# Kernel optimization log

Hardware: AMD Instinct MI355X
Metric: run time of the kernel (lower is better)

## Reference

```python
import jax, jax.numpy as jnp
import numpy as np

C = 64            # multiplicity of 0e and 1o in in_irreps
N_NODES = 20000
N_EDGES = 320000
RAD_DIM = 8
HID = 64
NUM_IRREPS_OUT = 4 * C   # 2C x 0e + 2C x 1o -> 256 scalar weights
AVG_NUM_NEIGHBORS = 16.0


def setup_inputs() -> dict:
    key = jax.random.key(0)
    ks = jax.random.split(key, 10)
    node_feats = jax.random.normal(ks[0], (N_NODES, C + 3 * C), jnp.float32)
    vectors = jax.random.normal(ks[1], (N_EDGES, 3), jnp.float32)
    radial_embedding = jax.random.normal(ks[2], (N_EDGES, RAD_DIM), jnp.float32)
    senders = jax.random.randint(ks[3], (N_EDGES,), 0, N_NODES, jnp.int32)
    receivers = jax.random.randint(ks[4], (N_EDGES,), 0, N_NODES, jnp.int32)
    # e3nn-style MLP params (no bias), forward scales by 1/sqrt(fan_in)
    W0 = jax.random.normal(ks[5], (RAD_DIM, HID), jnp.float32)
    W1 = jax.random.normal(ks[6], (HID, HID), jnp.float32)
    W2 = jax.random.normal(ks[7], (HID, HID), jnp.float32)
    W3 = jax.random.normal(ks[8], (HID, NUM_IRREPS_OUT), jnp.float32)
    return {"node_feats": node_feats, "vectors": vectors,
            "radial_embedding": radial_embedding, "senders": senders,
            "receivers": receivers, "W0": W0, "W1": W1, "W2": W2, "W3": W3}


def _mlp(x, W0, W1, W2, W3):
    # MultiLayerPerceptron with gradient_normalization=1.0: scale by 1/sqrt(fan_in)
    h = jax.nn.silu(x @ W0 / jnp.sqrt(jnp.asarray(W0.shape[0], x.dtype)))
    h = jax.nn.silu(h @ W1 / jnp.sqrt(jnp.asarray(HID, x.dtype)))
    h = jax.nn.silu(h @ W2 / jnp.sqrt(jnp.asarray(HID, x.dtype)))
    return h @ W3 / jnp.sqrt(jnp.asarray(HID, x.dtype))


def reference(node_feats, vectors, radial_embedding, senders, receivers, W0, W1, W2, W3):
    n = node_feats.shape[0]
    s = node_feats[:, :C]                      # [N, C]  0e block
    v = node_feats[:, C:].reshape(n, C, 3)     # [N, C, 3]  1o block
    s_e = s[senders]                           # gather  [E, C]
    v_e = v[senders]                           # gather  [E, C, 3]
    # spherical harmonics l=1 of -vectors, normalized input, component norm
    r = -vectors
    Y = jnp.sqrt(3.0) * r / jnp.linalg.norm(r, axis=-1, keepdims=True)  # [E, 3]
    # CG tensor product filtered to target irreps (0e + 1o):
    tp_v = s_e[:, :, None] * Y[:, None, :]                 # 0e x 1o -> 1o  [E,C,3]
    tp_s = jnp.einsum('eci,ei->ec', v_e, Y) / jnp.sqrt(3.0)  # 1o x 1o -> 0e  [E,C]
    msg_s = jnp.concatenate([s_e, tp_s], axis=-1)          # [E, 2C]
    msg_v = jnp.concatenate([v_e, tp_v], axis=1)           # [E, 2C, 3]
    # per-irrep MLP gate from radial embedding
    mix = _mlp(radial_embedding, W0, W1, W2, W3)           # [E, 4C]
    msg_s = msg_s * mix[:, :2 * C]
    msg_v = msg_v * mix[:, 2 * C:, None]
    # scatter-add into receivers
    out_s = jnp.zeros((n, 2 * C), msg_s.dtype).at[receivers].add(msg_s)
    out_v = jnp.zeros((n, 2 * C, 3), msg_v.dtype).at[receivers].add(msg_v)
    out = jnp.concatenate([out_s, out_v.reshape(n, 6 * C)], axis=-1)
    return out / AVG_NUM_NEIGHBORS                         # [N, 512]
```

## Files before the change

kernel.cpp:

```cpp
#include <hip/hip_runtime.h>

typedef __attribute__((ext_vector_type(8))) short bf16x8;
typedef __attribute__((ext_vector_type(4))) float f32x4;

static __device__ __forceinline__ unsigned short f2bf(float f) {
    unsigned int u = __float_as_uint(f);
    unsigned int r = (u + 0x7fffu + ((u >> 16) & 1u)) >> 16;
    return (unsigned short)r;
}
static __device__ __forceinline__ float bf2f(unsigned short h) {
    return __uint_as_float(((unsigned int)h) << 16);
}

#define WP_TOTAL 26624

__global__ __launch_bounds__(256) void zero_kernel(int* __restrict__ p, int n)
{
    int i = blockIdx.x * 256 + threadIdx.x;
    if (i < n) p[i] = 0;
}

__global__ __launch_bounds__(256) void prep_kernel(
    const float* __restrict__ W0, const float* __restrict__ W1,
    const float* __restrict__ W2, const float* __restrict__ W3,
    unsigned short* __restrict__ Wp,
    const int* __restrict__ recv, int* __restrict__ cnt, int E)
{
    int o = blockIdx.x * 256 + threadIdx.x;
    if (o < WP_TOTAL) {
        float val;
        if (o < 2048) {
            int nt = o >> 9, w = o & 511, lane = w >> 3, j = w & 7;
            int k = (lane >> 4) * 8 + j, n = nt * 16 + (lane & 15);
            val = (k < 8) ? W0[k * 64 + n] * 0.35355339059327373f : 0.f;
        } else if (o < 6144) {
            int oo = o - 2048, fid = oo >> 9, w = oo & 511, lane = w >> 3, j = w & 7;
            int nt = fid >> 1, ks = fid & 1;
            int k = ks * 32 + (lane >> 4) * 8 + j, n = nt * 16 + (lane & 15);
            val = W1[k * 64 + n] * 0.125f;
        } else if (o < 10240) {
            int oo = o - 6144, fid = oo >> 9, w = oo & 511, lane = w >> 3, j = w & 7;
            int nt = fid >> 1, ks = fid & 1;
            int k = ks * 32 + (lane >> 4) * 8 + j, n = nt * 16 + (lane & 15);
            val = W2[k * 64 + n] * 0.125f;
        } else {
            int oo = o - 10240, fid = oo >> 9, w = oo & 511, lane = w >> 3, j = w & 7;
            int nt = fid >> 1, ks = fid & 1;
            int k = ks * 32 + (lane >> 4) * 8 + j, n = nt * 16 + (lane & 15);
            val = W3[k * 256 + n] * 0.125f;
        }
        Wp[o] = f2bf(val);
    }
    if (o < E) atomicAdd(&cnt[recv[o]], 1);
}

__global__ __launch_bounds__(1024) void scan_kernel(const int* __restrict__ cnt,
                                                    int* __restrict__ off,
                                                    int* __restrict__ cursor, int N)
{
    __shared__ int wsum[16];
    const int t = threadIdx.x, lane = t & 63, wv = t >> 6;
    const int per = (N + 1023) / 1024;
    const int base = t * per;
    int s = 0;
    for (int i = 0; i < per; ++i) { int idx = base + i; if (idx < N) s += cnt[idx]; }
    int inc = s;
    #pragma unroll
    for (int d = 1; d < 64; d <<= 1) {
        int v = __shfl_up(inc, d, 64);
        if (lane >= d) inc += v;
    }
    if (lane == 63) wsum[wv] = inc;
    __syncthreads();
    if (t == 0) {
        int run = 0;
        #pragma unroll
        for (int w = 0; w < 16; ++w) { int v = wsum[w]; wsum[w] = run; run += v; }
    }
    __syncthreads();
    int run = wsum[wv] + inc - s;
    for (int i = 0; i < per; ++i) {
        int idx = base + i;
        if (idx < N) { off[idx] = run; cursor[idx] = run; run += cnt[idx]; }
    }
    if (t == 1023) off[N] = wsum[15] + inc;
}

__global__ __launch_bounds__(256) void fill_kernel(
    const int*   __restrict__ recv,
    const int*   __restrict__ senders,
    const float* __restrict__ vectors,
    int* __restrict__ cursor,
    int* __restrict__ edge_of,
    int* __restrict__ snd_pos,
    float4* __restrict__ Y4,
    int E)
{
    int i = blockIdx.x * 256 + threadIdx.x;
    if (i < E) {
        int p = atomicAdd(&cursor[recv[i]], 1);
        edge_of[p] = i;
        snd_pos[p] = senders[i];
        float r0 = -vectors[(size_t)i * 3 + 0];
        float r1 = -vectors[(size_t)i * 3 + 1];
        float r2 = -vectors[(size_t)i * 3 + 2];
        float inv = rsqrtf(r0 * r0 + r1 * r1 + r2 * r2);
        const float s3 = 1.7320508075688772f;
        Y4[p] = make_float4(s3 * r0 * inv, s3 * r1 * inv, s3 * r2 * inv, 0.f);
    }
}

__global__ __launch_bounds__(256) void mlp_pos_kernel(
    const float* __restrict__ radial,
    const int* __restrict__ edge_of,
    const unsigned short* __restrict__ Wp,
    unsigned short* __restrict__ mix,
    int E)
{
    __shared__ __align__(16) unsigned short sW[10240];
    __shared__ __align__(16) unsigned short sH[4][1024];
    __shared__ __align__(16) unsigned short sM[4][16 * 68];

    const int t = threadIdx.x;
    {
        int4* dst = (int4*)sW;
        const int4* src = (const int4*)Wp;
        #pragma unroll
        for (int i = 0; i < 5; ++i) dst[t + i * 256] = src[t + i * 256];
    }
    __syncthreads();

    const int wv = t >> 6, l = t & 63;
    const int lrow = l & 15, quad = l >> 4;
    const int p0 = blockIdx.x * 64 + wv * 16;
    if (p0 >= E) return;

    unsigned short* H = sH[wv];
    unsigned short* M = sM[wv];

    bf16x8 afr = {0, 0, 0, 0, 0, 0, 0, 0};
    if (quad == 0) {
        int i = p0 + lrow; if (i >= E) i = E - 1;
        int e = edge_of[i];
        const float* rr = radial + (size_t)e * 8;
        float4 ra = *(const float4*)rr;
        float4 rb = *(const float4*)(rr + 4);
        afr[0] = (short)f2bf(ra.x); afr[1] = (short)f2bf(ra.y);
        afr[2] = (short)f2bf(ra.z); afr[3] = (short)f2bf(ra.w);
        afr[4] = (short)f2bf(rb.x); afr[5] = (short)f2bf(rb.y);
        afr[6] = (short)f2bf(rb.z); afr[7] = (short)f2bf(rb.w);
    }
    #pragma unroll
    for (int nt = 0; nt < 4; ++nt) {
        bf16x8 b = *(const bf16x8*)(sW + nt * 512 + l * 8);
        f32x4 z = {0.f, 0.f, 0.f, 0.f};
        f32x4 cf = __builtin_amdgcn_mfma_f32_16x16x32_bf16(afr, b, z, 0, 0, 0);
        #pragma unroll
        for (int r = 0; r < 4; ++r) {
            float v = cf[r];
            float h = v / (1.f + __expf(-v));
            int er = quad * 4 + r;
            int f  = nt * 16 + lrow;
            H[er * 64 + (f ^ ((er & 7) << 3))] = f2bf(h);
        }
    }

    #pragma unroll 1
    for (int L = 0; L < 2; ++L) {
        const unsigned short* WL = sW + 2048 + L * 4096;
        bf16x8 a[2];
        #pragma unroll
        for (int ks = 0; ks < 2; ++ks)
            a[ks] = *(const bf16x8*)(H + lrow * 64 + ((ks * 32 + quad * 8) ^ ((lrow & 7) << 3)));
        f32x4 cf[4];
        #pragma unroll
        for (int nt = 0; nt < 4; ++nt) { f32x4 z = {0.f,0.f,0.f,0.f}; cf[nt] = z; }
        #pragma unroll
        for (int ks = 0; ks < 2; ++ks) {
            #pragma unroll
            for (int nt = 0; nt < 4; ++nt) {
                bf16x8 b = *(const bf16x8*)(WL + (nt * 2 + ks) * 512 + l * 8);
                cf[nt] = __builtin_amdgcn_mfma_f32_16x16x32_bf16(a[ks], b, cf[nt], 0, 0, 0);
            }
        }
        #pragma unroll
        for (int nt = 0; nt < 4; ++nt) {
            #pragma unroll
            for (int r = 0; r < 4; ++r) {
                float v = cf[nt][r];
                float h = v / (1.f + __expf(-v));
                int er = quad * 4 + r;
                int f  = nt * 16 + lrow;
                H[er * 64 + (f ^ ((er & 7) << 3))] = f2bf(h);
            }
        }
    }

    bf16x8 a3[2];
    #pragma unroll
    for (int ks = 0; ks < 2; ++ks)
        a3[ks] = *(const bf16x8*)(H + lrow * 64 + ((ks * 32 + quad * 8) ^ ((lrow & 7) << 3)));

    const unsigned short* W3 = Wp + 10240;
    #pragma unroll 1
    for (int g = 0; g < 4; ++g) {
        f32x4 cf[4];
        #pragma unroll
        for (int np = 0; np < 4; ++np) { f32x4 z = {0.f,0.f,0.f,0.f}; cf[np] = z; }
        #pragma unroll
        for (int ks = 0; ks < 2; ++ks) {
            #pragma unroll
            for (int np = 0; np < 4; ++np) {
                int nt = g * 4 + np;
                bf16x8 b = *(const bf16x8*)(W3 + (nt * 2 + ks) * 512 + l * 8);
                cf[np] = __builtin_amdgcn_mfma_f32_16x16x32_bf16(a3[ks], b, cf[np], 0, 0, 0);
            }
        }
        #pragma unroll
        for (int np = 0; np < 4; ++np) {
            int c2 = np * 16 + lrow;
            #pragma unroll
            for (int r = 0; r < 4; ++r)
                M[(quad * 4 + r) * 68 + c2] = f2bf(cf[np][r]);
        }
        #pragma unroll
        for (int i = 0; i < 4; ++i) {
            int ri = i * 4 + quad;
            ushort4 v = *(const ushort4*)&M[ri * 68 + lrow * 4];
            if (p0 + ri < E)
                *(ushort4*)&mix[(size_t)(p0 + ri) * 256 + g * 64 + lrow * 4] = v;
        }
    }
}

__global__ __launch_bounds__(256) void gather_kernel(
    const float* __restrict__ node_feats,
    const int*   __restrict__ snd_pos,
    const float4* __restrict__ Y4,
    const int*   __restrict__ off,
    const unsigned short* __restrict__ mix,
    float* __restrict__ out, int N)
{
    int wid  = threadIdx.x >> 6;
    int lane = threadIdx.x & 63;
    int n = blockIdx.x * 4 + wid;
    if (n >= N) return;

    int beg = off[n], end = off[n + 1];

    float a0 = 0.f, a1 = 0.f;
    float b0 = 0.f, b1 = 0.f, b2 = 0.f;
    float c0 = 0.f, c1 = 0.f, c2 = 0.f;

    const float is3 = 0.5773502691896258f;

    #pragma unroll 4
    for (int i = beg; i < end; ++i) {
        int snd  = snd_pos[i];
        float4 Y = Y4[i];

        const float* nf = node_feats + (size_t)snd * 256;
        float s_e = nf[lane];
        float v0  = nf[64 + lane * 3 + 0];
        float v1  = nf[64 + lane * 3 + 1];
        float v2  = nf[64 + lane * 3 + 2];

        const unsigned short* m = mix + (size_t)i * 256;
        float m0 = bf2f(m[lane]);
        float m1 = bf2f(m[64 + lane]);
        float m2 = bf2f(m[128 + lane]);
        float m3 = bf2f(m[192 + lane]);

        float tp_s = (v0 * Y.x + v1 * Y.y + v2 * Y.z) * is3;

        a0 += s_e * m0;
        a1 += tp_s * m1;
        b0 += v0 * m2; b1 += v1 * m2; b2 += v2 * m2;
        float sm = s_e * m3;
        c0 += Y.x * sm; c1 += Y.y * sm; c2 += Y.z * sm;
    }

    float* o = out + (size_t)n * 512;
    const float kk = 0.0625f;
    o[lane]      = a0 * kk;
    o[64 + lane] = a1 * kk;
    o[128 + lane * 3 + 0] = b0 * kk;
    o[128 + lane * 3 + 1] = b1 * kk;
    o[128 + lane * 3 + 2] = b2 * kk;
    o[320 + lane * 3 + 0] = c0 * kk;
    o[320 + lane * 3 + 1] = c1 * kk;
    o[320 + lane * 3 + 2] = c2 * kk;
}

#define HID 64
__global__ __launch_bounds__(256) void mlp_kernel(
    const float* __restrict__ radial,
    const float* __restrict__ W0g, const float* __restrict__ W1g,
    const float* __restrict__ W2g, const float* __restrict__ W3g,
    unsigned short* __restrict__ mix, int e1)
{
    __shared__ float  sHf[HID * 256];
    __shared__ float4 sW4[1024];

    const int t = threadIdx.x;
    const int e = blockIdx.x * 256 + t;
    const bool valid = e < e1;

    if (t < 128) sW4[t] = ((const float4*)W0g)[t];
    __syncthreads();

    float x[8];
    if (valid) {
        float4 ra = ((const float4*)radial)[(size_t)e * 2 + 0];
        float4 rb = ((const float4*)radial)[(size_t)e * 2 + 1];
        x[0]=ra.x; x[1]=ra.y; x[2]=ra.z; x[3]=ra.w;
        x[4]=rb.x; x[5]=rb.y; x[6]=rb.z; x[7]=rb.w;
    } else {
        #pragma unroll
        for (int k = 0; k < 8; ++k) x[k] = 0.f;
    }

    float acc[64];
    #pragma unroll
    for (int j = 0; j < 64; ++j) acc[j] = 0.f;
    #pragma unroll
    for (int k = 0; k < 8; ++k) {
        #pragma unroll
        for (int jq = 0; jq < 16; ++jq) {
            float4 w = sW4[k * 16 + jq];
            acc[jq*4+0] = fmaf(x[k], w.x, acc[jq*4+0]);
            acc[jq*4+1] = fmaf(x[k], w.y, acc[jq*4+1]);
            acc[jq*4+2] = fmaf(x[k], w.z, acc[jq*4+2]);
            acc[jq*4+3] = fmaf(x[k], w.w, acc[jq*4+3]);
        }
    }
    #pragma unroll
    for (int j = 0; j < 64; ++j) {
        float v = acc[j] * 0.35355339059327373f;
        sHf[j * 256 + t] = v / (1.f + __expf(-v));
    }
    __syncthreads();
    #pragma unroll
    for (int i = 0; i < 4; ++i) sW4[t + i * 256] = ((const float4*)W1g)[t + i * 256];
    __syncthreads();

    #pragma unroll
    for (int j = 0; j < 64; ++j) acc[j] = 0.f;
    #pragma unroll 2
    for (int k = 0; k < 64; ++k) {
        float hk = sHf[k * 256 + t];
        #pragma unroll
        for (int jq = 0; jq < 16; ++jq) {
            float4 w = sW4[k * 16 + jq];
            acc[jq*4+0] = fmaf(hk, w.x, acc[jq*4+0]);
            acc[jq*4+1] = fmaf(hk, w.y, acc[jq*4+1]);
            acc[jq*4+2] = fmaf(hk, w.z, acc[jq*4+2]);
            acc[jq*4+3] = fmaf(hk, w.w, acc[jq*4+3]);
        }
    }
    __syncthreads();
    #pragma unroll
    for (int i = 0; i < 4; ++i) sW4[t + i * 256] = ((const float4*)W2g)[t + i * 256];
    #pragma unroll
    for (int j = 0; j < 64; ++j) {
        float v = acc[j] * 0.125f;
        sHf[j * 256 + t] = v / (1.f + __expf(-v));
    }
    __syncthreads();

    #pragma unroll
    for (int j = 0; j < 64; ++j) acc[j] = 0.f;
    #pragma unroll 2
    for (int k = 0; k < 64; ++k) {
        float hk = sHf[k * 256 + t];
        #pragma unroll
        for (int jq = 0; jq < 16; ++jq) {
            float4 w = sW4[k * 16 + jq];
            acc[jq*4+0] = fmaf(hk, w.x, acc[jq*4+0]);
            acc[jq*4+1] = fmaf(hk, w.y, acc[jq*4+1]);
            acc[jq*4+2] = fmaf(hk, w.z, acc[jq*4+2]);
            acc[jq*4+3] = fmaf(hk, w.w, acc[jq*4+3]);
        }
    }
    __syncthreads();
    #pragma unroll
    for (int j = 0; j < 64; ++j) {
        float v = acc[j] * 0.125f;
        sHf[j * 256 + t] = v / (1.f + __expf(-v));
    }

    unsigned short* mrow = mix + (size_t)e * 256;
    #pragma unroll 1
    for (int jt = 0; jt < 4; ++jt) {
        #pragma unroll
        for (int i = 0; i < 4; ++i) {
            int m = t + i * 256;
            sW4[m] = ((const float4*)W3g)[(m >> 4) * 64 + jt * 16 + (m & 15)];
        }
        __syncthreads();

        #pragma unroll
        for (int j = 0; j < 64; ++j) acc[j] = 0.f;
        #pragma unroll 2
        for (int k = 0; k < 64; ++k) {
            float hk = sHf[k * 256 + t];
            #pragma unroll
            for (int jq = 0; jq < 16; ++jq) {
                float4 w = sW4[k * 16 + jq];
                acc[jq*4+0] = fmaf(hk, w.x, acc[jq*4+0]);
                acc[jq*4+1] = fmaf(hk, w.y, acc[jq*4+1]);
                acc[jq*4+2] = fmaf(hk, w.z, acc[jq*4+2]);
                acc[jq*4+3] = fmaf(hk, w.w, acc[jq*4+3]);
            }
        }
        if (valid) {
            #pragma unroll
            for (int j4 = 0; j4 < 16; ++j4) {
                ushort4 u;
                u.x = f2bf(acc[j4*4+0] * 0.125f);
                u.y = f2bf(acc[j4*4+1] * 0.125f);
                u.z = f2bf(acc[j4*4+2] * 0.125f);
                u.w = f2bf(acc[j4*4+3] * 0.125f);
                *reinterpret_cast<ushort4*>(&mrow[jt * 64 + j4 * 4]) = u;
            }
        }
        __syncthreads();
    }
}

__global__ __launch_bounds__(256) void scatter_kernel(
    const float* __restrict__ node_feats,
    const float* __restrict__ vectors,
    const int*   __restrict__ senders,
    const int*   __restrict__ receivers,
    const unsigned short* __restrict__ mix,
    float* __restrict__ out, int e0, int e1)
{
    int wid  = threadIdx.x >> 6;
    int lane = threadIdx.x & 63;
    int e = e0 + blockIdx.x * 4 + wid;
    if (e >= e1) return;

    int snd = senders[e];
    int rcv = receivers[e];

    float r0 = -vectors[(size_t)e * 3 + 0];
    float r1 = -vectors[(size_t)e * 3 + 1];
    float r2 = -vectors[(size_t)e * 3 + 2];
    float inv = rsqrtf(r0 * r0 + r1 * r1 + r2 * r2);
    float Y0 = 1.7320508075688772f * r0 * inv;
    float Y1 = 1.7320508075688772f * r1 * inv;
    float Y2 = 1.7320508075688772f * r2 * inv;

    const float* nf = node_feats + (size_t)snd * 256;
    float s_e = nf[lane];
    float v0 = nf[64 + lane * 3 + 0];
    float v1 = nf[64 + lane * 3 + 1];
    float v2 = nf[64 + lane * 3 + 2];

    float tp_s = (v0 * Y0 + v1 * Y1 + v2 * Y2) * 0.5773502691896258f;

    const unsigned short* m = mix + (size_t)(e - e0) * 256;
    float m0 = bf2f(m[lane]), m1 = bf2f(m[64 + lane]);
    float m2 = bf2f(m[128 + lane]), m3 = bf2f(m[192 + lane]);

    float* orow = out + (size_t)rcv * 512;
    const float kk = 0.0625f;
    atomicAdd(&orow[lane],      s_e  * m0 * kk);
    atomicAdd(&orow[64 + lane], tp_s * m1 * kk);
    float mv = m2 * kk;
    atomicAdd(&orow[128 + lane * 3 + 0], v0 * mv);
    atomicAdd(&orow[128 + lane * 3 + 1], v1 * mv);
    atomicAdd(&orow[128 + lane * 3 + 2], v2 * mv);
    float ms = s_e * m3 * kk;
    atomicAdd(&orow[320 + lane * 3 + 0], Y0 * ms);
    atomicAdd(&orow[320 + lane * 3 + 1], Y1 * ms);
    atomicAdd(&orow[320 + lane * 3 + 2], Y2 * ms);
}

extern "C" void kernel_launch(void* const* d_in, const int* in_sizes, int n_in,
                              void* d_out, int out_size, void* d_ws, size_t ws_size,
                              hipStream_t stream)
{
    const float* node_feats = (const float*)d_in[0];
    const float* vectors    = (const float*)d_in[1];
    const float* radial     = (const float*)d_in[2];
    const int*   senders    = (const int*)d_in[3];
    const int*   receivers  = (const int*)d_in[4];
    const float* W0         = (const float*)d_in[5];
    const float* W1         = (const float*)d_in[6];
    const float* W2         = (const float*)d_in[7];
    const float* W3         = (const float*)d_in[8];
    float* out = (float*)d_out;

    const int E = in_sizes[3];
    const int N = in_sizes[0] / 256;

    size_t mix_bytes = (size_t)E * 256 * sizeof(unsigned short);
    size_t mix_al    = (mix_bytes + 255) & ~(size_t)255;
    size_t int_bytes = (size_t)(N + (N + 1) + N + E + E) * sizeof(int);
    size_t int_al    = (int_bytes + 255) & ~(size_t)255;
    size_t y4_bytes  = (size_t)E * sizeof(float4);
    size_t y4_al     = (y4_bytes + 255) & ~(size_t)255;
    size_t wp_bytes  = (size_t)WP_TOTAL * sizeof(unsigned short);
    size_t need      = mix_al + int_al + y4_al + wp_bytes;

    if (ws_size >= need) {
        unsigned short* mix = (unsigned short*)d_ws;
        int* cnt      = (int*)((char*)d_ws + mix_al);
        int* off      = cnt + N;
        int* cursor   = off + (N + 1);
        int* edge_of  = cursor + N;
        int* snd_pos  = edge_of + E;
        float4* Y4    = (float4*)((char*)d_ws + mix_al + int_al);
        unsigned short* Wp = (unsigned short*)((char*)d_ws + mix_al + int_al + y4_al);

        zero_kernel<<<dim3((N + 255) / 256), dim3(256), 0, stream>>>(cnt, N);

        prep_kernel<<<dim3((E + 255) / 256), dim3(256), 0, stream>>>(
            W0, W1, W2, W3, Wp, receivers, cnt, E);
        scan_kernel<<<dim3(1), dim3(1024), 0, stream>>>(cnt, off, cursor, N);
        fill_kernel<<<dim3((E + 255) / 256), dim3(256), 0, stream>>>(
            receivers, senders, vectors, cursor, edge_of, snd_pos, Y4, E);

        mlp_pos_kernel<<<dim3((E + 63) / 64), dim3(256), 0, stream>>>(
            radial, edge_of, Wp, mix, E);

        gather_kernel<<<dim3((N + 3) / 4), dim3(256), 0, stream>>>(
            node_feats, snd_pos, Y4, off, mix, out, N);
    } else {
        hipMemsetAsync(d_out, 0, (size_t)out_size * sizeof(float), stream);
        size_t per_edge = 256 * sizeof(unsigned short);
        long long chunk_ll = (long long)(ws_size / per_edge);
        int chunk = (chunk_ll > E) ? E : (int)chunk_ll;
        chunk &= ~255;
        if (chunk <= 0) chunk = 256;
        unsigned short* mix = (unsigned short*)d_ws;
        for (int s = 0; s < E; s += chunk) {
            int eend = s + chunk; if (eend > E) eend = E;
            int ne = eend - s;
            mlp_kernel<<<dim3((ne + 255) / 256), dim3(256), 0, stream>>>(
                radial + (size_t)s * 8, W0, W1, W2, W3, mix, ne);
            scatter_kernel<<<dim3((ne + 3) / 4), dim3(256), 0, stream>>>(
                node_feats, vectors, senders, receivers, mix, out, s, eend);
        }
    }
}
```

Before: 225.8 us.

## Interleave node features and gate weights per channel for vectorized gather loads

Adds a kernel that repacks node features into one float4 per node and channel (scalar plus three vector components). The MLP now writes the four gate values for each channel contiguously as a ushort4, dropping the shared-memory staging buffer. The gather kernel then issues one 16-byte node load and one 8-byte gate load per lane instead of several strided scalar loads. The cost is an extra repack pass over node features and added workspace, and the MLP output stores become narrower and strided.

```diff
diff --git a/kernel.cpp b/kernel.cpp
--- a/kernel.cpp
+++ b/kernel.cpp
@@ -18,6 +18,18 @@
 {
     int i = blockIdx.x * 256 + threadIdx.x;
     if (i < n) p[i] = 0;
+}
+
+__global__ __launch_bounds__(256) void nf4_kernel(
+    const float* __restrict__ nf, float4* __restrict__ nf4, int N)
+{
+    int idx = blockIdx.x * 256 + threadIdx.x;
+    if (idx < N * 64) {
+        int n = idx >> 6, c = idx & 63;
+        const float* row = nf + (size_t)n * 256;
+        nf4[idx] = make_float4(row[c], row[64 + c * 3 + 0],
+                               row[64 + c * 3 + 1], row[64 + c * 3 + 2]);
+    }
 }
 
 __global__ __launch_bounds__(256) void prep_kernel(
@@ -114,12 +126,11 @@
     const float* __restrict__ radial,
     const int* __restrict__ edge_of,
     const unsigned short* __restrict__ Wp,
-    unsigned short* __restrict__ mix,
+    unsigned short* __restrict__ mix4,
     int E)
 {
     __shared__ __align__(16) unsigned short sW[10240];
     __shared__ __align__(16) unsigned short sH[4][1024];
-    __shared__ __align__(16) unsigned short sM[4][16 * 68];
 
     const int t = threadIdx.x;
     {
@@ -136,7 +147,6 @@
     if (p0 >= E) return;
 
     unsigned short* H = sH[wv];
-    unsigned short* M = sM[wv];
 
     bf16x8 afr = {0, 0, 0, 0, 0, 0, 0, 0};
     if (quad == 0) {
@@ -203,42 +213,39 @@
 
     const unsigned short* W3 = Wp + 10240;
     #pragma unroll 1
-    for (int g = 0; g < 4; ++g) {
+    for (int np = 0; np < 4; ++np) {
         f32x4 cf[4];
         #pragma unroll
-        for (int np = 0; np < 4; ++np) { f32x4 z = {0.f,0.f,0.f,0.f}; cf[np] = z; }
+        for (int g = 0; g < 4; ++g) { f32x4 z = {0.f,0.f,0.f,0.f}; cf[g] = z; }
         #pragma unroll
         for (int ks = 0; ks < 2; ++ks) {
             #pragma unroll
-            for (int np = 0; np < 4; ++np) {
+            for (int g = 0; g < 4; ++g) {
                 int nt = g * 4 + np;
                 bf16x8 b = *(const bf16x8*)(W3 + (nt * 2 + ks) * 512 + l * 8);
-                cf[np] = __builtin_amdgcn_mfma_f32_16x16x32_bf16(a3[ks], b, cf[np], 0, 0, 0);
+                cf[g] = __builtin_amdgcn_mfma_f32_16x16x32_bf16(a3[ks], b, cf[g], 0, 0, 0);
             }
         }
-        #pragma unroll
-        for (int np = 0; np < 4; ++np) {
-            int c2 = np * 16 + lrow;
-            #pragma unroll
-            for (int r = 0; r < 4; ++r)
-                M[(quad * 4 + r) * 68 + c2] = f2bf(cf[np][r]);
-        }
-        #pragma unroll
-        for (int i = 0; i < 4; ++i) {
-            int ri = i * 4 + quad;
-            ushort4 v = *(const ushort4*)&M[ri * 68 + lrow * 4];
-            if (p0 + ri < E)
-                *(ushort4*)&mix[(size_t)(p0 + ri) * 256 + g * 64 + lrow * 4] = v;
+        int c = np * 16 + lrow;
+        #pragma unroll
+        for (int r = 0; r < 4; ++r) {
+            int er = quad * 4 + r;
+            if (p0 + er < E) {
+                ushort4 u;
+                u.x = f2bf(cf[0][r]); u.y = f2bf(cf[1][r]);
+                u.z = f2bf(cf[2][r]); u.w = f2bf(cf[3][r]);
+                *(ushort4*)&mix4[((size_t)(p0 + er) * 64 + c) * 4] = u;
+            }
         }
     }
 }
 
 __global__ __launch_bounds__(256) void gather_kernel(
-    const float* __restrict__ node_feats,
+    const float4* __restrict__ nf4,
     const int*   __restrict__ snd_pos,
     const float4* __restrict__ Y4,
     const int*   __restrict__ off,
-    const unsigned short* __restrict__ mix,
+    const unsigned short* __restrict__ mix4,
     float* __restrict__ out, int N)
 {
     int wid  = threadIdx.x >> 6;
@@ -258,18 +265,11 @@
     for (int i = beg; i < end; ++i) {
         int snd  = snd_pos[i];
         float4 Y = Y4[i];
-
-        const float* nf = node_feats + (size_t)snd * 256;
-        float s_e = nf[lane];
-        float v0  = nf[64 + lane * 3 + 0];
-        float v1  = nf[64 + lane * 3 + 1];
-        float v2  = nf[64 + lane * 3 + 2];
-
-        const unsigned short* m = mix + (size_t)i * 256;
-        float m0 = bf2f(m[lane]);
-        float m1 = bf2f(m[64 + lane]);
-        float m2 = bf2f(m[128 + lane]);
-        float m3 = bf2f(m[192 + lane]);
+        float4 nv = nf4[(size_t)snd * 64 + lane];
+        ushort4 mv = *(const ushort4*)&mix4[((size_t)i * 64 + lane) * 4];
+
+        float s_e = nv.x, v0 = nv.y, v1 = nv.z, v2 = nv.w;
+        float m0 = bf2f(mv.x), m1 = bf2f(mv.y), m2 = bf2f(mv.z), m3 = bf2f(mv.w);
 
         float tp_s = (v0 * Y.x + v1 * Y.y + v2 * Y.z) * is3;
 
@@ -496,38 +496,43 @@
     const int E = in_sizes[3];
     const int N = in_sizes[0] / 256;
 
-    size_t mix_bytes = (size_t)E * 256 * sizeof(unsigned short);
+    size_t mix_bytes = (size_t)E * 64 * 4 * sizeof(unsigned short);
     size_t mix_al    = (mix_bytes + 255) & ~(size_t)255;
+    size_t nf4_bytes = (size_t)N * 64 * sizeof(float4);
+    size_t nf4_al    = (nf4_bytes + 255) & ~(size_t)255;
     size_t int_bytes = (size_t)(N + (N + 1) + N + E + E) * sizeof(int);
     size_t int_al    = (int_bytes + 255) & ~(size_t)255;
     size_t y4_bytes  = (size_t)E * sizeof(float4);
     size_t y4_al     = (y4_bytes + 255) & ~(size_t)255;
     size_t wp_bytes  = (size_t)WP_TOTAL * sizeof(unsigned short);
-    size_t need      = mix_al + int_al + y4_al + wp_bytes;
+    size_t need      = mix_al + nf4_al + int_al + y4_al + wp_bytes;
 
     if (ws_size >= need) {
-        unsigned short* mix = (unsigned short*)d_ws;
-        int* cnt      = (int*)((char*)d_ws + mix_al);
+        unsigned short* mix4 = (unsigned short*)d_ws;
+        float4* nf4   = (float4*)((char*)d_ws + mix_al);
+        int* cnt      = (int*)((char*)d_ws + mix_al + nf4_al);
         int* off      = cnt + N;
         int* cursor   = off + (N + 1);
         int* edge_of  = cursor + N;
         int* snd_pos  = edge_of + E;
-        float4* Y4    = (float4*)((char*)d_ws + mix_al + int_al);
-        unsigned short* Wp = (unsigned short*)((char*)d_ws + mix_al + int_al + y4_al);
+        float4* Y4    = (float4*)((char*)d_ws + mix_al + nf4_al + int_al);
+        unsigned short* Wp = (unsigned short*)((char*)d_ws + mix_al + nf4_al + int_al + y4_al);
 
         zero_kernel<<<dim3((N + 255) / 256), dim3(256), 0, stream>>>(cnt, N);
 
         prep_kernel<<<dim3((E + 255) / 256), dim3(256), 0, stream>>>(
             W0, W1, W2, W3, Wp, receivers, cnt, E);
+        nf4_kernel<<<dim3((N * 64 + 255) / 256), dim3(256), 0, stream>>>(
+            node_feats, nf4, N);
         scan_kernel<<<dim3(1), dim3(1024), 0, stream>>>(cnt, off, cursor, N);
         fill_kernel<<<dim3((E + 255) / 256), dim3(256), 0, stream>>>(
             receivers, senders, vectors, cursor, edge_of, snd_pos, Y4, E);
 
         mlp_pos_kernel<<<dim3((E + 63) / 64), dim3(256), 0, stream>>>(
-            radial, edge_of, Wp, mix, E);
+            radial, edge_of, Wp, mix4, E);
 
         gather_kernel<<<dim3((N + 3) / 4), dim3(256), 0, stream>>>(
-            node_feats, snd_pos, Y4, off, mix, out, N);
+            nf4, snd_pos, Y4, off, mix4, out, N);
     } else {
         hipMemsetAsync(d_out, 0, (size_t)out_size * sizeof(float), stream);
         size_t per_edge = 256 * sizeof(unsigned short);
```

Measured after the change: 231.3 us. +2.4%, slower.
